# Optimization experiments

Measured on AMD Instinct MI355X. Metric: run time of the kernel, lower is better.

The kernel has to match this reference:

```python
import jax, jax.numpy as jnp
import numpy as np
from jax import lax

# ---- static config (matches init_kwargs: input_shape=(1,64,64), num_classes=2) ----
C, H, W = 1, 64, 64
NUM_CLASSES = 2
DIM_CAPS = 8          # primary capsule dim
NUM_PRIM = 32         # primary capsule types
OUT_DIM = 16          # class capsule dim
NUM_ROUTING = 3
HP = (H - 9) // 2 + 1  # 28  (9x9 conv, stride 2, no pad)
WP = (W - 9) // 2 + 1  # 28
IN_CAPS = NUM_PRIM * HP * WP  # 25088
TEMP_CH = 256 // H    # 4  channels after re-viewing temporal output
B = 32


def conv1d(x, w, b, pad):
    y = lax.conv_general_dilated(x, w, (1,), [(pad, pad)],
                                 dimension_numbers=('NCH', 'OIH', 'NCH'))
    return y + b[None, :, None]


def conv2d(x, w, b, stride, pad):
    y = lax.conv_general_dilated(x, w, (stride, stride), [(pad, pad), (pad, pad)],
                                 dimension_numbers=('NCHW', 'OIHW', 'NCHW'))
    return y + b[None, :, None, None]


def squash_vec(u):
    # proper capsule squash over last (dim_caps) axis -- used by PrimaryCapsule
    sn = jnp.sum(u * u, axis=-1, keepdims=True)
    return sn * u / ((1.0 + sn) * jnp.sqrt(sn + 1e-8))


def squash_elem(v):
    # RoutingCapsule squash: torch applies it over a trailing SINGLETON dim,
    # so it is elementwise: v^2 * v / ((1+v^2) * sqrt(v^2 + 1e-8))
    sn = v * v
    return sn * v / ((1.0 + sn) * jnp.sqrt(sn + 1e-8))


def setup_inputs() -> dict:
    key = jax.random.key(0)
    ks = jax.random.split(key, 20)
    s = 0.05
    inp = {
        'x':    jax.random.normal(ks[0], (B, C, H, W), dtype=jnp.float32),
        # temporal Conv1d stack (true in_channels = C*H = 64)
        'w_t1': jax.random.normal(ks[1], (64, C * H, 5), jnp.float32) * s,
        'b_t1': jnp.zeros((64,), jnp.float32),
        'w_t2': jax.random.normal(ks[2], (128, 64, 5), jnp.float32) * s,
        'b_t2': jnp.zeros((128,), jnp.float32),
        'w_t3': jax.random.normal(ks[3], (256, 128, 5), jnp.float32) * s,
        'b_t3': jnp.zeros((256,), jnp.float32),
        # spectral Conv2d stack
        'w_s1': jax.random.normal(ks[4], (64, C, 3, 3), jnp.float32) * s,
        'b_s1': jnp.zeros((64,), jnp.float32),
        'w_s2': jax.random.normal(ks[5], (128, 64, 3, 3), jnp.float32) * s,
        'b_s2': jnp.zeros((128,), jnp.float32),
        'w_s3': jax.random.normal(ks[6], (256, 128, 3, 3), jnp.float32) * s,
        'b_s3': jnp.zeros((256,), jnp.float32),
        # fusion 1x1 conv (in = 256/H + 256 = 260)
        'w_f':  jax.random.normal(ks[7], (256, TEMP_CH + 256, 1, 1), jnp.float32) * s,
        'b_f':  jnp.zeros((256,), jnp.float32),
        # primary capsule 9x9 stride-2 conv (out = 32*8 = 256)
        'w_p':  jax.random.normal(ks[8], (NUM_PRIM * DIM_CAPS, 256, 9, 9), jnp.float32) * s,
        'b_p':  jnp.zeros((NUM_PRIM * DIM_CAPS,), jnp.float32),
        # routing weight (torch: (1, in_caps, out_caps, out_dim, in_dim); leading 1 dropped)
        'w_r':  jax.random.normal(ks[9], (IN_CAPS, NUM_CLASSES, OUT_DIM, DIM_CAPS), jnp.float32) * s,
    }
    return inp


def reference(x, w_t1, b_t1, w_t2, b_t2, w_t3, b_t3,
              w_s1, b_s1, w_s2, b_s2, w_s3, b_s3,
              w_f, b_f, w_p, b_p, w_r):
    bsz = x.shape[0]
    # temporal branch: (B, C*H, W) -> Conv1d x3 -> (B, 256, W) -> (B, 256/H, H, W)
    xt = x.reshape(bsz, C * H, W)
    t = jax.nn.relu(conv1d(xt, w_t1, b_t1, 2))
    t = jax.nn.relu(conv1d(t, w_t2, b_t2, 2))
    t = jax.nn.relu(conv1d(t, w_t3, b_t3, 2))
    t = t.reshape(bsz, TEMP_CH, H, W)
    # spectral branch
    sp = jax.nn.relu(conv2d(x, w_s1, b_s1, 1, 1))
    sp = jax.nn.relu(conv2d(sp, w_s2, b_s2, 1, 1))
    sp = jax.nn.relu(conv2d(sp, w_s3, b_s3, 1, 1))
    # fuse
    fused = jnp.concatenate([t, sp], axis=1)          # (B, 260, H, W)
    fused = conv2d(fused, w_f, b_f, 1, 0)             # (B, 256, H, W)
    # primary capsules
    p = conv2d(fused, w_p, b_p, 2, 0)                 # (B, 256, HP, WP)
    p = p.reshape(bsz, NUM_PRIM, DIM_CAPS, HP * WP)
    p = jnp.transpose(p, (0, 1, 3, 2)).reshape(bsz, IN_CAPS, DIM_CAPS)
    u = squash_vec(p)                                 # (B, in_caps, 8)
    # dynamic routing
    u_hat = jnp.einsum('iodk,bik->biod', w_r, u)      # (B, in_caps, out_caps, out_dim)
    b_ij = jnp.zeros((bsz, IN_CAPS, NUM_CLASSES), dtype=u_hat.dtype)
    v = None
    for it in range(NUM_ROUTING):
        c = jax.nn.softmax(b_ij, axis=2)              # over out_caps
        s_j = jnp.einsum('bio,biod->bod', c, u_hat)   # (B, out_caps, out_dim)
        v = squash_elem(s_j)                          # elementwise (singleton-dim squash)
        if it < NUM_ROUTING - 1:
            b_ij = b_ij + jnp.einsum('biod,bod->bio', u_hat, v)
    # class_probs = (class_caps**2).sum(-1)**0.5 over a SINGLETON dim -> |v|
    return (v * v) ** 0.5                             # (B, num_classes, out_dim)
```

## Files before the change

### kernel.cpp

```cpp
#include <hip/hip_runtime.h>
#include <math.h>


#define BSZ 32

typedef unsigned short u16;
using bf16x8 = __attribute__((ext_vector_type(8))) short;
using f16x8 = __attribute__((ext_vector_type(8))) _Float16;
using f32x4 = __attribute__((ext_vector_type(4))) float;

__device__ inline u16 f2bf(float f) {
  union { float f; unsigned u; } v; v.f = f;
  unsigned r = v.u + 0x7FFF + ((v.u >> 16) & 1);
  return (u16)(r >> 16);
}
__device__ inline float bf2f(u16 h) {
  union { unsigned u; float f; } v; v.u = ((unsigned)h) << 16;
  return v.f;
}
__device__ inline u16 f2h(float f) {
  union { _Float16 h; u16 u; } v; v.h = (_Float16)f;
  return v.u;
}
__device__ inline float h2f(u16 b) {
  union { u16 u; _Float16 h; } v; v.u = b;
  return (float)v.h;
}

__global__ __launch_bounds__(256) void conv1d_relu_k(
    const float* __restrict__ in, const float* __restrict__ w,
    const float* __restrict__ bias, float* __restrict__ out, int CI, int CO) {
  int idx = blockIdx.x * 256 + threadIdx.x;
  int total = BSZ * CO * 64;
  if (idx >= total) return;
  int x = idx & 63;
  int co = (idx >> 6) % CO;
  int b = idx / (64 * CO);
  const float* ip = in + (size_t)b * CI * 64;
  const float* wp = w + (size_t)co * CI * 5;
  float acc = bias[co];
  for (int ci = 0; ci < CI; ++ci) {
    const float* ir = ip + ci * 64;
    const float* wr_ = wp + ci * 5;
#pragma unroll
    for (int k = 0; k < 5; ++k) {
      int xx = x + k - 2;
      if (xx >= 0 && xx < 64) acc += ir[xx] * wr_[k];
    }
  }
  out[idx] = fmaxf(acc, 0.f);
}

template <int CI, int CIC>
__global__ __launch_bounds__(256) void conv3x3_relu_k(
    const float* __restrict__ in, const float* __restrict__ w,
    const float* __restrict__ bias, float* __restrict__ out, int CO) {
  __shared__ float in_t[CIC][18][20];
  __shared__ float w_t[CIC][16][12];
  int t = threadIdx.x;
  int co_l = t & 15;
  int g = t >> 4;
  int gy = g >> 2, gx = g & 3;
  int y0 = (blockIdx.x >> 2) * 16, x0 = (blockIdx.x & 3) * 16;
  int co = blockIdx.y * 16 + co_l;
  int b = blockIdx.z;
  float acc[16];
#pragma unroll
  for (int i = 0; i < 16; ++i) acc[i] = 0.f;

  for (int cib = 0; cib < CI / CIC; ++cib) {
    int ci0 = cib * CIC;
    for (int s = t; s < CIC * 324; s += 256) {
      int ci = s / 324;
      int r = s - ci * 324;
      int iy = r / 18, ix = r - iy * 18;
      int gyy = y0 + iy - 1, gxx = x0 + ix - 1;
      float v = 0.f;
      if (gyy >= 0 && gyy < 64 && gxx >= 0 && gxx < 64)
        v = in[((size_t)b * CI + ci0 + ci) * 4096 + gyy * 64 + gxx];
      in_t[ci][iy][ix] = v;
    }
    for (int s = t; s < CIC * 144; s += 256) {
      int ci = s / 144;
      int r = s - ci * 144;
      int cw = r / 9, k = r - cw * 9;
      w_t[ci][cw][k] = w[((size_t)(blockIdx.y * 16 + cw) * CI + ci0 + ci) * 9 + k];
    }
    __syncthreads();
    for (int ci = 0; ci < CIC; ++ci) {
      float wv[9];
#pragma unroll
      for (int k = 0; k < 9; ++k) wv[k] = w_t[ci][co_l][k];
      float pin[36];
#pragma unroll
      for (int r6 = 0; r6 < 6; ++r6)
#pragma unroll
        for (int c6 = 0; c6 < 6; ++c6)
          pin[r6 * 6 + c6] = in_t[ci][4 * gy + r6][4 * gx + c6];
#pragma unroll
      for (int py = 0; py < 4; ++py)
#pragma unroll
        for (int px = 0; px < 4; ++px) {
          float s_ = acc[py * 4 + px];
#pragma unroll
          for (int ky = 0; ky < 3; ++ky)
#pragma unroll
            for (int kx = 0; kx < 3; ++kx)
              s_ += pin[(py + ky) * 6 + (px + kx)] * wv[ky * 3 + kx];
          acc[py * 4 + px] = s_;
        }
    }
    __syncthreads();
  }
  float bv = bias[co];
#pragma unroll
  for (int py = 0; py < 4; ++py)
#pragma unroll
    for (int px = 0; px < 4; ++px)
      out[((size_t)b * CO + co) * 4096 + (size_t)(y0 + 4 * gy + py) * 64 +
          (x0 + 4 * gx + px)] = fmaxf(acc[py * 4 + px] + bv, 0.f);
}

__global__ __launch_bounds__(256) void transpose_wf_k(const float* __restrict__ wf,
                                                      float* __restrict__ wfT) {
  int idx = blockIdx.x * 256 + threadIdx.x;
  if (idx >= 256 * 260) return;
  int co = idx / 260, c = idx - co * 260;
  wfT[c * 256 + co] = wf[idx];
}

__global__ __launch_bounds__(256) void transpose_wp_k(const float* __restrict__ wp,
                                                      u16* __restrict__ wth,
                                                      u16* __restrict__ wtl) {
  int s = blockIdx.x;
  int g = s / 81, t = s - g * 81;
  int co = threadIdx.x;
  u16 th[32], tl[32];
#pragma unroll
  for (int c = 0; c < 32; ++c) {
    float f = wp[((size_t)co * 256 + g * 32 + c) * 81 + t];
    u16 h = f2h(f);
    th[c] = h;
    tl[c] = f2h(f - h2f(h));
  }
  ushort4* dh = (ushort4*)(wth + ((size_t)s * 256 + co) * 32);
  ushort4* dl = (ushort4*)(wtl + ((size_t)s * 256 + co) * 32);
#pragma unroll
  for (int q = 0; q < 8; ++q) {
    dh[q] = make_ushort4(th[4 * q], th[4 * q + 1], th[4 * q + 2], th[4 * q + 3]);
    dl[q] = make_ushort4(tl[4 * q], tl[4 * q + 1], tl[4 * q + 2], tl[4 * q + 3]);
  }
}

template <int CO, int NCHUNK>
__global__ __launch_bounds__(256) void transpose_w3_k(const float* __restrict__ w,
                                                      u16* __restrict__ wh,
                                                      u16* __restrict__ wl) {
  int tab = blockIdx.x;
  int g = tab / 9, tap = tab - g * 9;
  int co = threadIdx.x;
  if (co >= CO) return;
  constexpr int CI = NCHUNK * 32;
  u16 th[32], tl[32];
#pragma unroll
  for (int c = 0; c < 32; ++c) {
    float f = w[((size_t)co * CI + g * 32 + c) * 9 + tap];
    u16 h = f2bf(f);
    th[c] = h;
    tl[c] = f2bf(f - bf2f(h));
  }
  ushort4* dh = (ushort4*)(wh + ((size_t)tab * CO + co) * 32);
  ushort4* dl = (ushort4*)(wl + ((size_t)tab * CO + co) * 32);
#pragma unroll
  for (int q = 0; q < 8; ++q) {
    dh[q] = make_ushort4(th[4 * q], th[4 * q + 1], th[4 * q + 2], th[4 * q + 3]);
    dl[q] = make_ushort4(tl[4 * q], tl[4 * q + 1], tl[4 * q + 2], tl[4 * q + 3]);
  }
}

template <int WMG, int WNG, int NCHUNK, int CO>
__global__ __launch_bounds__(512) void conv3x3_mfma_k(const float* __restrict__ in,
                                                      const u16* __restrict__ Wh,
                                                      const u16* __restrict__ Wl,
                                                      const float* __restrict__ bias,
                                                      float* __restrict__ out) {
  constexpr int CI = NCHUNK * 32;
  constexpr int ROWS = WMG + 2;
  __shared__ __align__(16) char lds_a[ROWS * 66 * 80];
  const int tid = threadIdx.x;
  const int b = blockIdx.y;
  const int y0 = blockIdx.x * WMG;
  const int w = tid >> 6, l = tid & 63;
  const int wm = w / WNG, wn = w % WNG;
  const int kb = l >> 4, il = l & 15;

  int abase[4];
#pragma unroll
  for (int mb = 0; mb < 4; ++mb) {
    int lp = (wm * 4 + mb) * 16 + il;
    int ly = lp >> 6, lx = lp & 63;
    abase[mb] = (ly * 66 + lx) * 80 + kb * 16;
  }
  int boff[4];
#pragma unroll
  for (int nbi = 0; nbi < 4; ++nbi)
    boff[nbi] = ((wn * 4 + nbi) * 16 + il) * 64 + kb * 16;

  f32x4 acc[4][4];
#pragma unroll
  for (int mb = 0; mb < 4; ++mb)
#pragma unroll
    for (int nbi = 0; nbi < 4; ++nbi) {
      f32x4 z = {0.f, 0.f, 0.f, 0.f};
      acc[mb][nbi] = z;
    }

  const float* Fb = in + (size_t)b * CI * 4096;
  const char* WhB = (const char*)Wh;
  const char* WlB = (const char*)Wl;

  auto stageA = [&](int g, int plane) {
    const float* src = Fb + (size_t)g * 32 * 4096;
    for (int s = tid; s < ROWS * 66 * 8; s += 512) {
      int ciq = s & 7;
      int rest = s >> 3;
      int r = rest / 66, x = rest - r * 66;
      int row = y0 - 1 + r, col = x - 1;
      float a0 = 0.f, a1 = 0.f, a2 = 0.f, a3 = 0.f;
      if (row >= 0 && row < 64 && col >= 0 && col < 64) {
        const float* p = src + (size_t)(ciq * 4) * 4096 + row * 64 + col;
        a0 = p[0];
        a1 = p[4096];
        a2 = p[8192];
        a3 = p[12288];
      }
      u16 e0, e1, e2, e3;
      if (plane == 0) {
        e0 = f2bf(a0); e1 = f2bf(a1); e2 = f2bf(a2); e3 = f2bf(a3);
      } else {
        u16 h0 = f2bf(a0), h1 = f2bf(a1), h2 = f2bf(a2), h3 = f2bf(a3);
        e0 = f2bf(a0 - bf2f(h0)); e1 = f2bf(a1 - bf2f(h1));
        e2 = f2bf(a2 - bf2f(h2)); e3 = f2bf(a3 - bf2f(h3));
      }
      *(ushort4*)(lds_a + (r * 66 + x) * 80 + ciq * 8) = make_ushort4(e0, e1, e2, e3);
    }
  };

  for (int g = 0; g < NCHUNK; ++g) {
    __syncthreads();
    stageA(g, 0);
    __syncthreads();
#pragma unroll
    for (int tap = 0; tap < 9; ++tap) {
      const char* pb = WhB + (size_t)(g * 9 + tap) * (CO * 64);
      const char* pl = WlB + (size_t)(g * 9 + tap) * (CO * 64);
      bf16x8 bh[4], bl[4];
#pragma unroll
      for (int nbi = 0; nbi < 4; ++nbi) {
        bh[nbi] = *(const bf16x8*)(pb + boff[nbi]);
        bl[nbi] = *(const bf16x8*)(pl + boff[nbi]);
      }
      int ky = tap / 3, kx = tap - ky * 3;
      int toff = (ky * 66 + kx) * 80;
      bf16x8 av[4];
#pragma unroll
      for (int mb = 0; mb < 4; ++mb)
        av[mb] = *(const bf16x8*)(lds_a + abase[mb] + toff);
#pragma unroll
      for (int mb = 0; mb < 4; ++mb)
#pragma unroll
        for (int nbi = 0; nbi < 4; ++nbi) {
          acc[mb][nbi] = __builtin_amdgcn_mfma_f32_16x16x32_bf16(
              av[mb], bh[nbi], acc[mb][nbi], 0, 0, 0);
          acc[mb][nbi] = __builtin_amdgcn_mfma_f32_16x16x32_bf16(
              av[mb], bl[nbi], acc[mb][nbi], 0, 0, 0);
        }
    }
    __syncthreads();
    stageA(g, 1);
    __syncthreads();
#pragma unroll
    for (int tap = 0; tap < 9; ++tap) {
      const char* pb = WhB + (size_t)(g * 9 + tap) * (CO * 64);
      bf16x8 bh[4];
#pragma unroll
      for (int nbi = 0; nbi < 4; ++nbi)
        bh[nbi] = *(const bf16x8*)(pb + boff[nbi]);
      int ky = tap / 3, kx = tap - ky * 3;
      int toff = (ky * 66 + kx) * 80;
      bf16x8 av[4];
#pragma unroll
      for (int mb = 0; mb < 4; ++mb)
        av[mb] = *(const bf16x8*)(lds_a + abase[mb] + toff);
#pragma unroll
      for (int mb = 0; mb < 4; ++mb)
#pragma unroll
        for (int nbi = 0; nbi < 4; ++nbi)
          acc[mb][nbi] = __builtin_amdgcn_mfma_f32_16x16x32_bf16(
              av[mb], bh[nbi], acc[mb][nbi], 0, 0, 0);
    }
  }

  const int p0 = y0 * 64;
#pragma unroll
  for (int mb = 0; mb < 4; ++mb) {
    int pixb = p0 + (wm * 4 + mb) * 16 + kb * 4;
#pragma unroll
    for (int nbi = 0; nbi < 4; ++nbi) {
      int co = (wn * 4 + nbi) * 16 + il;
      float bv_ = bias[co];
      f32x4 a = acc[mb][nbi];
      float4 o = make_float4(fmaxf(a[0] + bv_, 0.f), fmaxf(a[1] + bv_, 0.f),
                             fmaxf(a[2] + bv_, 0.f), fmaxf(a[3] + bv_, 0.f));
      *(float4*)(out + (size_t)(b * CO + co) * 4096 + pixb) = o;
    }
  }
}

__global__ __launch_bounds__(256) void fuse1x1_k(const float* __restrict__ t3,
                                                 const float* __restrict__ wfT,
                                                 const float* __restrict__ bf,
                                                 float* __restrict__ a) {
  __shared__ float in_t[260][32];
  int t = threadIdx.x;
  int b = blockIdx.x >> 7;
  int p0 = (blockIdx.x & 127) * 32;
  for (int s = t; s < 260 * 32; s += 256) {
    int c = s >> 5, pp = s & 31;
    float v;
    if (c < 4)
      v = t3[(size_t)b * 16384 + c * 4096 + p0 + pp];
    else
      v = a[((size_t)b * 256 + (c - 4)) * 4096 + p0 + pp];
    in_t[c][pp] = v;
  }
  __syncthreads();
  int co = t;
  float acc[32];
#pragma unroll
  for (int pp = 0; pp < 32; ++pp) acc[pp] = 0.f;
  for (int c = 0; c < 260; ++c) {
    float wv = wfT[c * 256 + co];
#pragma unroll
    for (int pp = 0; pp < 32; ++pp) acc[pp] += wv * in_t[c][pp];
  }
  float bv = bf[co];
#pragma unroll
  for (int pp = 0; pp < 32; ++pp)
    a[((size_t)b * 256 + co) * 4096 + p0 + pp] = acc[pp] + bv;
}

__global__ __launch_bounds__(1024) void conv9x9_mfma_k(const float* __restrict__ fused,
                                                       const u16* __restrict__ WTh,
                                                       const u16* __restrict__ WTl,
                                                       const float* __restrict__ bias,
                                                       float* __restrict__ praw) {
  constexpr int APLANE = 19 * 32 * 80;
  __shared__ __align__(16) char lds_a[2 * APLANE];
  const int tid = threadIdx.x;
  const int b = blockIdx.y, tile = blockIdx.x;
  const int p0 = tile * 128;
  const int oy0 = p0 / 28;
  const int w = tid >> 6, l = tid & 63;
  const int wm = w >> 3, wn = w & 7;
  const int kb = l >> 4, il = l & 15;

  int abase[4];
#pragma unroll
  for (int mb = 0; mb < 4; ++mb) {
    int p = p0 + (wm * 4 + mb) * 16 + il;
    int oy = p / 28, ox = p - oy * 28;
    abase[mb] = (2 * (oy - oy0)) * 2560 + ox * 80 + kb * 16;
  }
  int boff[2];
#pragma unroll
  for (int nbi = 0; nbi < 2; ++nbi)
    boff[nbi] = (wn * 32 + nbi * 16 + il) * 64 + kb * 16;

  f32x4 acc[4][2];
#pragma unroll
  for (int mb = 0; mb < 4; ++mb)
#pragma unroll
    for (int nbi = 0; nbi < 2; ++nbi) {
      f32x4 z = {0.f, 0.f, 0.f, 0.f};
      acc[mb][nbi] = z;
    }

  const float* Fb = fused + (size_t)b * 256 * 4096;
  const char* WhB = (const char*)WTh;
  const char* WlB = (const char*)WTl;

  auto stageA = [&](int g) {
    const float* src = Fb + (size_t)g * 32 * 4096;
    for (int s = tid; s < 19 * 63 * 8; s += 1024) {
      int ciq = s / 1197;
      int rem = s - ciq * 1197;
      int r = rem / 63, t63 = rem - r * 63;
      int x2 = (t63 < 32) ? 2 * t63 : 2 * (t63 - 32) + 1;
      int iy = 2 * oy0 + r;
      float a0 = 0.f, a1 = 0.f, a2 = 0.f, a3 = 0.f;
      if (iy < 64) {
        const float* pp0 = src + (size_t)(ciq * 4) * 4096 + iy * 64 + x2;
        a0 = pp0[0];
        a1 = pp0[4096];
        a2 = pp0[8192];
        a3 = pp0[12288];
      }
      u16 e0 = f2h(a0), e1 = f2h(a1), e2 = f2h(a2), e3 = f2h(a3);
      int off = (x2 & 1) * APLANE + (r * 32 + (x2 >> 1)) * 80 + ciq * 8;
      *(ushort4*)(lds_a + off) = make_ushort4(e0, e1, e2, e3);
    }
  };

  for (int g = 0; g < 8; ++g) {
    __syncthreads();
    stageA(g);
    __syncthreads();
#pragma unroll 3
    for (int t = 0; t < 81; ++t) {
      const char* pb = WhB + (size_t)(g * 81 + t) * 16384;
      const char* pl = WlB + (size_t)(g * 81 + t) * 16384;
      f16x8 bh[2], bl[2];
#pragma unroll
      for (int nbi = 0; nbi < 2; ++nbi) {
        bh[nbi] = *(const f16x8*)(pb + boff[nbi]);
        bl[nbi] = *(const f16x8*)(pl + boff[nbi]);
      }
      int ky = t / 9, kx = t - ky * 9;
      int toff = (kx & 1) * APLANE + ky * 2560 + (kx >> 1) * 80;
      f16x8 av[4];
#pragma unroll
      for (int mb = 0; mb < 4; ++mb)
        av[mb] = *(const f16x8*)(lds_a + abase[mb] + toff);
#pragma unroll
      for (int mb = 0; mb < 4; ++mb)
#pragma unroll
        for (int nbi = 0; nbi < 2; ++nbi) {
          acc[mb][nbi] = __builtin_amdgcn_mfma_f32_16x16x32_f16(
              av[mb], bh[nbi], acc[mb][nbi], 0, 0, 0);
          acc[mb][nbi] = __builtin_amdgcn_mfma_f32_16x16x32_f16(
              av[mb], bl[nbi], acc[mb][nbi], 0, 0, 0);
        }
    }
  }

#pragma unroll
  for (int mb = 0; mb < 4; ++mb) {
    int pixb = p0 + (wm * 4 + mb) * 16 + kb * 4;
    if (pixb < 784) {
#pragma unroll
      for (int nbi = 0; nbi < 2; ++nbi) {
        int co = wn * 32 + nbi * 16 + il;
        float bv_ = bias[co];
        f32x4 a = acc[mb][nbi];
        float4 o = make_float4(a[0] + bv_, a[1] + bv_, a[2] + bv_, a[3] + bv_);
        *(float4*)(praw + (size_t)(b * 256 + co) * 784 + pixb) = o;
      }
    }
  }
}

__global__ __launch_bounds__(256) void squash_caps_k(const float* __restrict__ p,
                                                     float* __restrict__ u) {
  int idx = blockIdx.x * 256 + threadIdx.x;
  if (idx >= BSZ * 25088) return;
  int b = idx / 25088;
  int cap = idx - b * 25088;
  int prim = cap / 784, pix = cap - prim * 784;
  const float* pp = p + ((size_t)b * 256 + prim * 8) * 784 + pix;
  float x[8];
  float sn = 0.f;
#pragma unroll
  for (int d = 0; d < 8; ++d) {
    x[d] = pp[(size_t)d * 784];
    sn += x[d] * x[d];
  }
  float scale = sn / ((1.f + sn) * sqrtf(sn + 1e-8f));
  float4 r0 = {x[0] * scale, x[1] * scale, x[2] * scale, x[3] * scale};
  float4 r1 = {x[4] * scale, x[5] * scale, x[6] * scale, x[7] * scale};
  float4* dst = (float4*)(u + (size_t)idx * 8);
  dst[0] = r0;
  dst[1] = r1;
}

__global__ __launch_bounds__(256) void uhat_k(const float* __restrict__ u,
                                              const float* __restrict__ w_r,
                                              float* __restrict__ u_hat) {
  int i = blockIdx.x * 256 + threadIdx.x;
  int b = blockIdx.y;
  const float4* up = (const float4*)(u + ((size_t)b * 25088 + i) * 8);
  float4 ua = up[0], ub = up[1];
  const float4* wr = (const float4*)(w_r + (size_t)i * 256);
  float res[32];
#pragma unroll
  for (int od = 0; od < 32; ++od) {
    float4 wa = wr[od * 2], wb = wr[od * 2 + 1];
    res[od] = wa.x * ua.x + wa.y * ua.y + wa.z * ua.z + wa.w * ua.w +
              wb.x * ub.x + wb.y * ub.y + wb.z * ub.z + wb.w * ub.w;
  }
  float4* dst = (float4*)(u_hat + ((size_t)b * 25088 + i) * 32);
#pragma unroll
  for (int q = 0; q < 8; ++q)
    dst[q] = make_float4(res[4 * q], res[4 * q + 1], res[4 * q + 2], res[4 * q + 3]);
}

__global__ __launch_bounds__(256) void route_sj_k(const float* __restrict__ u_hat,
                                                  const float* __restrict__ b_ij,
                                                  float* __restrict__ sj_part, int iter) {
  int b = blockIdx.x;
  int seg = blockIdx.y;
  int t = threadIdx.x;
  float acc[32];
#pragma unroll
  for (int j = 0; j < 32; ++j) acc[j] = 0.f;
  int i0 = seg * 3136;
  for (int i = i0 + t; i < i0 + 3136; i += 256) {
    float c0 = 0.5f, c1 = 0.5f;
    if (iter > 0) {
      float b0 = b_ij[((size_t)b * 25088 + i) * 2 + 0];
      float b1 = b_ij[((size_t)b * 25088 + i) * 2 + 1];
      float m = fmaxf(b0, b1);
      float e0 = expf(b0 - m), e1 = expf(b1 - m);
      float inv = 1.f / (e0 + e1);
      c0 = e0 * inv;
      c1 = e1 * inv;
    }
    const float4* uh = (const float4*)(u_hat + ((size_t)b * 25088 + i) * 32);
#pragma unroll
    for (int q = 0; q < 4; ++q) {
      float4 va = uh[q];
      acc[4 * q + 0] += c0 * va.x;
      acc[4 * q + 1] += c0 * va.y;
      acc[4 * q + 2] += c0 * va.z;
      acc[4 * q + 3] += c0 * va.w;
      float4 vb = uh[4 + q];
      acc[16 + 4 * q + 0] += c1 * vb.x;
      acc[16 + 4 * q + 1] += c1 * vb.y;
      acc[16 + 4 * q + 2] += c1 * vb.z;
      acc[16 + 4 * q + 3] += c1 * vb.w;
    }
  }
#pragma unroll
  for (int j = 0; j < 32; ++j) {
    acc[j] += __shfl_down(acc[j], 32);
    acc[j] += __shfl_down(acc[j], 16);
    acc[j] += __shfl_down(acc[j], 8);
    acc[j] += __shfl_down(acc[j], 4);
    acc[j] += __shfl_down(acc[j], 2);
    acc[j] += __shfl_down(acc[j], 1);
  }
  __shared__ float red[4][32];
  int wave = t >> 6, lane = t & 63;
  if (lane == 0) {
#pragma unroll
    for (int j = 0; j < 32; ++j) red[wave][j] = acc[j];
  }
  __syncthreads();
  if (t < 32) {
    float s = red[0][t] + red[1][t] + red[2][t] + red[3][t];
    sj_part[((size_t)b * 8 + seg) * 32 + t] = s;
  }
}

__global__ __launch_bounds__(256) void route_fin_k(const float* __restrict__ sj_part,
                                                   float* __restrict__ v,
                                                   float* __restrict__ out, int final_it) {
  int idx = blockIdx.x * 256 + threadIdx.x;
  if (idx >= BSZ * 32) return;
  int b = idx >> 5, j = idx & 31;
  float s = 0.f;
#pragma unroll
  for (int seg = 0; seg < 8; ++seg) s += sj_part[((size_t)b * 8 + seg) * 32 + j];
  float sn = s * s;
  float vv = sn * s / ((1.f + sn) * sqrtf(sn + 1e-8f));
  v[idx] = vv;
  if (final_it) out[idx] = fabsf(vv);
}

__global__ __launch_bounds__(256) void route_upd_k(const float* __restrict__ u_hat,
                                                   const float* __restrict__ v,
                                                   float* __restrict__ b_ij, int first) {
  int i = blockIdx.x * 256 + threadIdx.x;
  int b = blockIdx.y;
  const float4* uh = (const float4*)(u_hat + ((size_t)b * 25088 + i) * 32);
  const float4* vp = (const float4*)(v + b * 32);
  float e0 = 0.f, e1 = 0.f;
#pragma unroll
  for (int q = 0; q < 4; ++q) {
    float4 a = uh[q], wv = vp[q];
    e0 += a.x * wv.x + a.y * wv.y + a.z * wv.z + a.w * wv.w;
    float4 a2 = uh[4 + q], w2 = vp[4 + q];
    e1 += a2.x * w2.x + a2.y * w2.y + a2.z * w2.z + a2.w * w2.w;
  }
  size_t o = ((size_t)b * 25088 + i) * 2;
  if (first) {
    b_ij[o + 0] = e0;
    b_ij[o + 1] = e1;
  } else {
    b_ij[o + 0] += e0;
    b_ij[o + 1] += e1;
  }
}

extern "C" void kernel_launch(void* const* d_in, const int* in_sizes, int n_in,
                              void* d_out, int out_size, void* d_ws, size_t ws_size,
                              hipStream_t stream) {
  (void)in_sizes; (void)n_in; (void)out_size;
  const float* x    = (const float*)d_in[0];
  const float* w_t1 = (const float*)d_in[1];
  const float* b_t1 = (const float*)d_in[2];
  const float* w_t2 = (const float*)d_in[3];
  const float* b_t2 = (const float*)d_in[4];
  const float* w_t3 = (const float*)d_in[5];
  const float* b_t3 = (const float*)d_in[6];
  const float* w_s1 = (const float*)d_in[7];
  const float* b_s1 = (const float*)d_in[8];
  const float* w_s2 = (const float*)d_in[9];
  const float* b_s2 = (const float*)d_in[10];
  const float* w_s3 = (const float*)d_in[11];
  const float* b_s3 = (const float*)d_in[12];
  const float* w_f  = (const float*)d_in[13];
  const float* b_f  = (const float*)d_in[14];
  const float* w_p  = (const float*)d_in[15];
  const float* b_p  = (const float*)d_in[16];
  const float* w_r  = (const float*)d_in[17];
  float* out = (float*)d_out;

  char* ws = (char*)d_ws;
  if (ws_size < 238854144ull) return;
  float* fused = (float*)(ws + 0);
  float* uhat  = (float*)(ws + 0);
  float* s2q   = (float*)(ws + 134217728);
  float* praw  = (float*)(ws + 134217728);
  float* u     = (float*)(ws + 159907840);
  float* b_ij  = (float*)(ws + 185597952);
  float* s1    = (float*)(ws + 201326592);
  float* t1    = (float*)(ws + 201326592);
  float* t2    = (float*)(ws + 201850880);
  float* t3    = (float*)(ws + 202899456);
  u16*   wTh   = (u16*)  (ws + 204996608);
  u16*   wTl   = (u16*)  (ws + 215613440);
  u16*   w3a_h = (u16*)  (ws + 234881024);
  u16*   w3a_l = (u16*)  (ws + 235028480);
  u16*   w3b_h = (u16*)  (ws + 235175936);
  u16*   w3b_l = (u16*)  (ws + 235765760);
  float* wfT   = (float*)(ws + 236355584);
  float* sjp   = (float*)(ws + 236621824);
  float* vbuf  = (float*)(ws + 236654592);

  transpose_w3_k<128, 2><<<18, 256, 0, stream>>>(w_s2, w3a_h, w3a_l);
  transpose_w3_k<256, 4><<<36, 256, 0, stream>>>(w_s3, w3b_h, w3b_l);
  transpose_wf_k<<<261, 256, 0, stream>>>(w_f, wfT);

  conv3x3_relu_k<1, 1><<<dim3(16, 4, BSZ), 256, 0, stream>>>(x, w_s1, b_s1, s1, 64);
  conv3x3_mfma_k<4, 2, 2, 128><<<dim3(16, BSZ), 512, 0, stream>>>(s1, w3a_h, w3a_l, b_s2, s2q);

  conv1d_relu_k<<<512, 256, 0, stream>>>(x, w_t1, b_t1, t1, 64, 64);
  conv1d_relu_k<<<1024, 256, 0, stream>>>(t1, w_t2, b_t2, t2, 64, 128);
  conv1d_relu_k<<<2048, 256, 0, stream>>>(t2, w_t3, b_t3, t3, 128, 256);
  transpose_wp_k<<<648, 256, 0, stream>>>(w_p, wTh, wTl);

  conv3x3_mfma_k<2, 4, 4, 256><<<dim3(32, BSZ), 512, 0, stream>>>(s2q, w3b_h, w3b_l, b_s3, fused);

  fuse1x1_k<<<4096, 256, 0, stream>>>(t3, wfT, b_f, fused);

  conv9x9_mfma_k<<<dim3(7, BSZ), 1024, 0, stream>>>(fused, wTh, wTl, b_p, praw);
  squash_caps_k<<<3136, 256, 0, stream>>>(praw, u);

  uhat_k<<<dim3(98, BSZ), 256, 0, stream>>>(u, w_r, uhat);

  route_sj_k<<<dim3(BSZ, 8), 256, 0, stream>>>(uhat, b_ij, sjp, 0);
  route_fin_k<<<4, 256, 0, stream>>>(sjp, vbuf, out, 0);
  route_upd_k<<<dim3(98, BSZ), 256, 0, stream>>>(uhat, vbuf, b_ij, 1);

  route_sj_k<<<dim3(BSZ, 8), 256, 0, stream>>>(uhat, b_ij, sjp, 1);
  route_fin_k<<<4, 256, 0, stream>>>(sjp, vbuf, out, 0);
  route_upd_k<<<dim3(98, BSZ), 256, 0, stream>>>(uhat, vbuf, b_ij, 0);

  route_sj_k<<<dim3(BSZ, 8), 256, 0, stream>>>(uhat, b_ij, sjp, 2);
  route_fin_k<<<4, 256, 0, stream>>>(sjp, vbuf, out, 1);
}
```

Before: 1.774 ms.

## Move 1x1 fuse conv to split-bf16 MFMA and fuse routing update into s_j pass

Replaces the scalar FP32 1x1 fusion convolution with an MFMA kernel that splits activations and weights into bf16 high/low parts and uses three products to keep near-FP32 accuracy. The weight transpose now emits packed bf16 hi/lo tiles. Separately, the routing logit update is folded into the next s_j reduction pass, so u_hat is read once per iteration instead of twice. It also specialises the first s_j pass to the uniform 0.5 coupling. The costs are a small precision loss from dropping the low-times-low term and in-place reads and writes of the fused buffer inside the GEMM.

```diff
diff --git a/kernel.cpp b/kernel.cpp
--- a/kernel.cpp
+++ b/kernel.cpp
@@ -121,12 +121,27 @@
           (x0 + 4 * gx + px)] = fmaxf(acc[py * 4 + px] + bv, 0.f);
 }
 
-__global__ __launch_bounds__(256) void transpose_wf_k(const float* __restrict__ wf,
-                                                      float* __restrict__ wfT) {
-  int idx = blockIdx.x * 256 + threadIdx.x;
-  if (idx >= 256 * 260) return;
-  int co = idx / 260, c = idx - co * 260;
-  wfT[c * 256 + co] = wf[idx];
+__global__ __launch_bounds__(256) void transpose_wf1_k(const float* __restrict__ wf,
+                                                       u16* __restrict__ wh,
+                                                       u16* __restrict__ wl) {
+  int c = blockIdx.x;
+  int co = threadIdx.x;
+  u16 th[32], tl[32];
+#pragma unroll
+  for (int j = 0; j < 32; ++j) {
+    int lc = c * 32 + j;
+    float f = (lc < 260) ? wf[(size_t)co * 260 + lc] : 0.f;
+    u16 h = f2bf(f);
+    th[j] = h;
+    tl[j] = f2bf(f - bf2f(h));
+  }
+  ushort4* dh = (ushort4*)(wh + ((size_t)c * 256 + co) * 32);
+  ushort4* dl = (ushort4*)(wl + ((size_t)c * 256 + co) * 32);
+#pragma unroll
+  for (int q = 0; q < 8; ++q) {
+    dh[q] = make_ushort4(th[4 * q], th[4 * q + 1], th[4 * q + 2], th[4 * q + 3]);
+    dl[q] = make_ushort4(tl[4 * q], tl[4 * q + 1], tl[4 * q + 2], tl[4 * q + 3]);
+  }
 }
 
 __global__ __launch_bounds__(256) void transpose_wp_k(const float* __restrict__ wp,
@@ -317,37 +332,105 @@
   }
 }
 
-__global__ __launch_bounds__(256) void fuse1x1_k(const float* __restrict__ t3,
-                                                 const float* __restrict__ wfT,
-                                                 const float* __restrict__ bf,
-                                                 float* __restrict__ a) {
-  __shared__ float in_t[260][32];
-  int t = threadIdx.x;
-  int b = blockIdx.x >> 7;
-  int p0 = (blockIdx.x & 127) * 32;
-  for (int s = t; s < 260 * 32; s += 256) {
-    int c = s >> 5, pp = s & 31;
-    float v;
-    if (c < 4)
-      v = t3[(size_t)b * 16384 + c * 4096 + p0 + pp];
-    else
-      v = a[((size_t)b * 256 + (c - 4)) * 4096 + p0 + pp];
-    in_t[c][pp] = v;
-  }
-  __syncthreads();
-  int co = t;
-  float acc[32];
-#pragma unroll
-  for (int pp = 0; pp < 32; ++pp) acc[pp] = 0.f;
-  for (int c = 0; c < 260; ++c) {
-    float wv = wfT[c * 256 + co];
-#pragma unroll
-    for (int pp = 0; pp < 32; ++pp) acc[pp] += wv * in_t[c][pp];
-  }
-  float bv = bf[co];
-#pragma unroll
-  for (int pp = 0; pp < 32; ++pp)
-    a[((size_t)b * 256 + co) * 4096 + p0 + pp] = acc[pp] + bv;
+__global__ __launch_bounds__(512) void fuse_mfma_k(const float* __restrict__ t3,
+                                                   const u16* __restrict__ Wh,
+                                                   const u16* __restrict__ Wl,
+                                                   const float* __restrict__ bf,
+                                                   float* __restrict__ a) {
+  constexpr int APL = 128 * 80;
+  __shared__ __align__(16) char lds_a[2 * APL];
+  const int tid = threadIdx.x;
+  const int b = blockIdx.y;
+  const int p0 = blockIdx.x * 128;
+  const int w = tid >> 6, l = tid & 63;
+  const int wm = w >> 2, wn = w & 3;
+  const int kb = l >> 4, il = l & 15;
+
+  int abase[4];
+#pragma unroll
+  for (int mb = 0; mb < 4; ++mb)
+    abase[mb] = ((wm * 4 + mb) * 16 + il) * 80 + kb * 16;
+  int boff[4];
+#pragma unroll
+  for (int nbi = 0; nbi < 4; ++nbi)
+    boff[nbi] = ((wn * 4 + nbi) * 16 + il) * 64 + kb * 16;
+
+  f32x4 acc[4][4];
+#pragma unroll
+  for (int mb = 0; mb < 4; ++mb)
+#pragma unroll
+    for (int nbi = 0; nbi < 4; ++nbi) {
+      f32x4 z = {0.f, 0.f, 0.f, 0.f};
+      acc[mb][nbi] = z;
+    }
+
+  const char* WhB = (const char*)Wh;
+  const char* WlB = (const char*)Wl;
+
+  auto stageAB = [&](int c) {
+    for (int s = tid; s < 128 * 8; s += 512) {
+      int ciq = s & 7, px = s >> 3;
+      int pg = p0 + px;
+      u16 eh[4], el[4];
+#pragma unroll
+      for (int q = 0; q < 4; ++q) {
+        int lc = c * 32 + ciq * 4 + q;
+        float f = 0.f;
+        if (lc < 4)
+          f = t3[(size_t)b * 16384 + lc * 4096 + pg];
+        else if (lc < 260)
+          f = a[((size_t)b * 256 + (lc - 4)) * 4096 + pg];
+        u16 h = f2bf(f);
+        eh[q] = h;
+        el[q] = f2bf(f - bf2f(h));
+      }
+      *(ushort4*)(lds_a + px * 80 + ciq * 8) = make_ushort4(eh[0], eh[1], eh[2], eh[3]);
+      *(ushort4*)(lds_a + APL + px * 80 + ciq * 8) =
+          make_ushort4(el[0], el[1], el[2], el[3]);
+    }
+  };
+
+  for (int c = 0; c < 9; ++c) {
+    __syncthreads();
+    stageAB(c);
+    __syncthreads();
+    bf16x8 bh[4], bl[4];
+#pragma unroll
+    for (int nbi = 0; nbi < 4; ++nbi) {
+      bh[nbi] = *(const bf16x8*)(WhB + (size_t)c * 16384 + boff[nbi]);
+      bl[nbi] = *(const bf16x8*)(WlB + (size_t)c * 16384 + boff[nbi]);
+    }
+    bf16x8 avh[4], avl[4];
+#pragma unroll
+    for (int mb = 0; mb < 4; ++mb) {
+      avh[mb] = *(const bf16x8*)(lds_a + abase[mb]);
+      avl[mb] = *(const bf16x8*)(lds_a + APL + abase[mb]);
+    }
+#pragma unroll
+    for (int mb = 0; mb < 4; ++mb)
+#pragma unroll
+      for (int nbi = 0; nbi < 4; ++nbi) {
+        acc[mb][nbi] = __builtin_amdgcn_mfma_f32_16x16x32_bf16(
+            avh[mb], bh[nbi], acc[mb][nbi], 0, 0, 0);
+        acc[mb][nbi] = __builtin_amdgcn_mfma_f32_16x16x32_bf16(
+            avh[mb], bl[nbi], acc[mb][nbi], 0, 0, 0);
+        acc[mb][nbi] = __builtin_amdgcn_mfma_f32_16x16x32_bf16(
+            avl[mb], bh[nbi], acc[mb][nbi], 0, 0, 0);
+      }
+  }
+
+#pragma unroll
+  for (int mb = 0; mb < 4; ++mb) {
+    int pixb = p0 + (wm * 4 + mb) * 16 + kb * 4;
+#pragma unroll
+    for (int nbi = 0; nbi < 4; ++nbi) {
+      int co = (wn * 4 + nbi) * 16 + il;
+      float bv_ = bf[co];
+      f32x4 v = acc[mb][nbi];
+      float4 o = make_float4(v[0] + bv_, v[1] + bv_, v[2] + bv_, v[3] + bv_);
+      *(float4*)(a + (size_t)(b * 256 + co) * 4096 + pixb) = o;
+    }
+  }
 }
 
 __global__ __launch_bounds__(1024) void conv9x9_mfma_k(const float* __restrict__ fused,
@@ -452,8 +535,8 @@
       for (int nbi = 0; nbi < 2; ++nbi) {
         int co = wn * 32 + nbi * 16 + il;
         float bv_ = bias[co];
-        f32x4 a = acc[mb][nbi];
-        float4 o = make_float4(a[0] + bv_, a[1] + bv_, a[2] + bv_, a[3] + bv_);
+        f32x4 v = acc[mb][nbi];
+        float4 o = make_float4(v[0] + bv_, v[1] + bv_, v[2] + bv_, v[3] + bv_);
         *(float4*)(praw + (size_t)(b * 256 + co) * 784 + pixb) = o;
       }
     }
@@ -505,8 +588,7 @@
 }
 
 __global__ __launch_bounds__(256) void route_sj_k(const float* __restrict__ u_hat,
-                                                  const float* __restrict__ b_ij,
-                                                  float* __restrict__ sj_part, int iter) {
+                                                  float* __restrict__ sj_part) {
   int b = blockIdx.x;
   int seg = blockIdx.y;
   int t = threadIdx.x;
@@ -515,29 +597,19 @@
   for (int j = 0; j < 32; ++j) acc[j] = 0.f;
   int i0 = seg * 3136;
   for (int i = i0 + t; i < i0 + 3136; i += 256) {
-    float c0 = 0.5f, c1 = 0.5f;
-    if (iter > 0) {
-      float b0 = b_ij[((size_t)b * 25088 + i) * 2 + 0];
-      float b1 = b_ij[((size_t)b * 25088 + i) * 2 + 1];
-      float m = fmaxf(b0, b1);
-      float e0 = expf(b0 - m), e1 = expf(b1 - m);
-      float inv = 1.f / (e0 + e1);
-      c0 = e0 * inv;
-      c1 = e1 * inv;
-    }
     const float4* uh = (const float4*)(u_hat + ((size_t)b * 25088 + i) * 32);
 #pragma unroll
     for (int q = 0; q < 4; ++q) {
       float4 va = uh[q];
-      acc[4 * q + 0] += c0 * va.x;
-      acc[4 * q + 1] += c0 * va.y;
-      acc[4 * q + 2] += c0 * va.z;
-      acc[4 * q + 3] += c0 * va.w;
+      acc[4 * q + 0] += 0.5f * va.x;
+      acc[4 * q + 1] += 0.5f * va.y;
+      acc[4 * q + 2] += 0.5f * va.z;
+      acc[4 * q + 3] += 0.5f * va.w;
       float4 vb = uh[4 + q];
-      acc[16 + 4 * q + 0] += c1 * vb.x;
-      acc[16 + 4 * q + 1] += c1 * vb.y;
-      acc[16 + 4 * q + 2] += c1 * vb.z;
-      acc[16 + 4 * q + 3] += c1 * vb.w;
+      acc[16 + 4 * q + 0] += 0.5f * vb.x;
+      acc[16 + 4 * q + 1] += 0.5f * vb.y;
+      acc[16 + 4 * q + 2] += 0.5f * vb.z;
+      acc[16 + 4 * q + 3] += 0.5f * vb.w;
     }
   }
 #pragma unroll
@@ -562,6 +634,82 @@
   }
 }
 
+__global__ __launch_bounds__(256) void route_fsj_k(const float* __restrict__ u_hat,
+                                                   const float* __restrict__ v,
+                                                   float* __restrict__ b_ij,
+                                                   float* __restrict__ sj_part, int first) {
+  int b = blockIdx.x;
+  int seg = blockIdx.y;
+  int t = threadIdx.x;
+  float4 vp[8];
+  const float4* vv = (const float4*)(v + b * 32);
+#pragma unroll
+  for (int q = 0; q < 8; ++q) vp[q] = vv[q];
+  float acc[32];
+#pragma unroll
+  for (int j = 0; j < 32; ++j) acc[j] = 0.f;
+  int i0 = seg * 3136;
+  for (int i = i0 + t; i < i0 + 3136; i += 256) {
+    const float4* uhp = (const float4*)(u_hat + ((size_t)b * 25088 + i) * 32);
+    float4 uh[8];
+#pragma unroll
+    for (int q = 0; q < 8; ++q) uh[q] = uhp[q];
+    float e0 = 0.f, e1 = 0.f;
+#pragma unroll
+    for (int q = 0; q < 4; ++q) {
+      e0 += uh[q].x * vp[q].x + uh[q].y * vp[q].y + uh[q].z * vp[q].z + uh[q].w * vp[q].w;
+      e1 += uh[4 + q].x * vp[4 + q].x + uh[4 + q].y * vp[4 + q].y +
+            uh[4 + q].z * vp[4 + q].z + uh[4 + q].w * vp[4 + q].w;
+    }
+    size_t o = ((size_t)b * 25088 + i) * 2;
+    float b0, b1;
+    if (first) {
+      b0 = e0;
+      b1 = e1;
+      b_ij[o + 0] = e0;
+      b_ij[o + 1] = e1;
+    } else {
+      b0 = b_ij[o + 0] + e0;
+      b1 = b_ij[o + 1] + e1;
+    }
+    float m = fmaxf(b0, b1);
+    float x0 = expf(b0 - m), x1 = expf(b1 - m);
+    float inv = 1.f / (x0 + x1);
+    float c0 = x0 * inv, c1 = x1 * inv;
+#pragma unroll
+    for (int q = 0; q < 4; ++q) {
+      acc[4 * q + 0] += c0 * uh[q].x;
+      acc[4 * q + 1] += c0 * uh[q].y;
+      acc[4 * q + 2] += c0 * uh[q].z;
+      acc[4 * q + 3] += c0 * uh[q].w;
+      acc[16 + 4 * q + 0] += c1 * uh[4 + q].x;
+      acc[16 + 4 * q + 1] += c1 * uh[4 + q].y;
+      acc[16 + 4 * q + 2] += c1 * uh[4 + q].z;
+      acc[16 + 4 * q + 3] += c1 * uh[4 + q].w;
+    }
+  }
+#pragma unroll
+  for (int j = 0; j < 32; ++j) {
+    acc[j] += __shfl_down(acc[j], 32);
+    acc[j] += __shfl_down(acc[j], 16);
+    acc[j] += __shfl_down(acc[j], 8);
+    acc[j] += __shfl_down(acc[j], 4);
+    acc[j] += __shfl_down(acc[j], 2);
+    acc[j] += __shfl_down(acc[j], 1);
+  }
+  __shared__ float red[4][32];
+  int wave = t >> 6, lane = t & 63;
+  if (lane == 0) {
+#pragma unroll
+    for (int j = 0; j < 32; ++j) red[wave][j] = acc[j];
+  }
+  __syncthreads();
+  if (t < 32) {
+    float s = red[0][t] + red[1][t] + red[2][t] + red[3][t];
+    sj_part[((size_t)b * 8 + seg) * 32 + t] = s;
+  }
+}
+
 __global__ __launch_bounds__(256) void route_fin_k(const float* __restrict__ sj_part,
                                                    float* __restrict__ v,
                                                    float* __restrict__ out, int final_it) {
@@ -575,31 +723,6 @@
   float vv = sn * s / ((1.f + sn) * sqrtf(sn + 1e-8f));
   v[idx] = vv;
   if (final_it) out[idx] = fabsf(vv);
-}
-
-__global__ __launch_bounds__(256) void route_upd_k(const float* __restrict__ u_hat,
-                                                   const float* __restrict__ v,
-                                                   float* __restrict__ b_ij, int first) {
-  int i = blockIdx.x * 256 + threadIdx.x;
-  int b = blockIdx.y;
-  const float4* uh = (const float4*)(u_hat + ((size_t)b * 25088 + i) * 32);
-  const float4* vp = (const float4*)(v + b * 32);
-  float e0 = 0.f, e1 = 0.f;
-#pragma unroll
-  for (int q = 0; q < 4; ++q) {
-    float4 a = uh[q], wv = vp[q];
-    e0 += a.x * wv.x + a.y * wv.y + a.z * wv.z + a.w * wv.w;
-    float4 a2 = uh[4 + q], w2 = vp[4 + q];
-    e1 += a2.x * w2.x + a2.y * w2.y + a2.z * w2.z + a2.w * w2.w;
-  }
-  size_t o = ((size_t)b * 25088 + i) * 2;
-  if (first) {
-    b_ij[o + 0] = e0;
-    b_ij[o + 1] = e1;
-  } else {
-    b_ij[o + 0] += e0;
-    b_ij[o + 1] += e1;
-  }
 }
 
 extern "C" void kernel_launch(void* const* d_in, const int* in_sizes, int n_in,
@@ -644,13 +767,14 @@
   u16*   w3a_l = (u16*)  (ws + 235028480);
   u16*   w3b_h = (u16*)  (ws + 235175936);
   u16*   w3b_l = (u16*)  (ws + 235765760);
-  float* wfT   = (float*)(ws + 236355584);
-  float* sjp   = (float*)(ws + 236621824);
-  float* vbuf  = (float*)(ws + 236654592);
+  u16*   wf1_h = (u16*)  (ws + 236355584);
+  u16*   wf1_l = (u16*)  (ws + 236503040);
+  float* sjp   = (float*)(ws + 236650496);
+  float* vbuf  = (float*)(ws + 236683264);
 
   transpose_w3_k<128, 2><<<18, 256, 0, stream>>>(w_s2, w3a_h, w3a_l);
   transpose_w3_k<256, 4><<<36, 256, 0, stream>>>(w_s3, w3b_h, w3b_l);
-  transpose_wf_k<<<261, 256, 0, stream>>>(w_f, wfT);
+  transpose_wf1_k<<<9, 256, 0, stream>>>(w_f, wf1_h, wf1_l);
 
   conv3x3_relu_k<1, 1><<<dim3(16, 4, BSZ), 256, 0, stream>>>(x, w_s1, b_s1, s1, 64);
   conv3x3_mfma_k<4, 2, 2, 128><<<dim3(16, BSZ), 512, 0, stream>>>(s1, w3a_h, w3a_l, b_s2, s2q);
@@ -662,21 +786,17 @@
 
   conv3x3_mfma_k<2, 4, 4, 256><<<dim3(32, BSZ), 512, 0, stream>>>(s2q, w3b_h, w3b_l, b_s3, fused);
 
-  fuse1x1_k<<<4096, 256, 0, stream>>>(t3, wfT, b_f, fused);
+  fuse_mfma_k<<<dim3(32, BSZ), 512, 0, stream>>>(t3, wf1_h, wf1_l, b_f, fused);
 
   conv9x9_mfma_k<<<dim3(7, BSZ), 1024, 0, stream>>>(fused, wTh, wTl, b_p, praw);
   squash_caps_k<<<3136, 256, 0, stream>>>(praw, u);
 
   uhat_k<<<dim3(98, BSZ), 256, 0, stream>>>(u, w_r, uhat);
 
-  route_sj_k<<<dim3(BSZ, 8), 256, 0, stream>>>(uhat, b_ij, sjp, 0);
+  route_sj_k<<<dim3(BSZ, 8), 256, 0, stream>>>(uhat, sjp);
   route_fin_k<<<4, 256, 0, stream>>>(sjp, vbuf, out, 0);
-  route_upd_k<<<dim3(98, BSZ), 256, 0, stream>>>(uhat, vbuf, b_ij, 1);
-
-  route_sj_k<<<dim3(BSZ, 8), 256, 0, stream>>>(uhat, b_ij, sjp, 1);
+  route_fsj_k<<<dim3(BSZ, 8), 256, 0, stream>>>(uhat, vbuf, b_ij, sjp, 1);
   route_fin_k<<<4, 256, 0, stream>>>(sjp, vbuf, out, 0);
-  route_upd_k<<<dim3(98, BSZ), 256, 0, stream>>>(uhat, vbuf, b_ij, 0);
-
-  route_sj_k<<<dim3(BSZ, 8), 256, 0, stream>>>(uhat, b_ij, sjp, 2);
+  route_fsj_k<<<dim3(BSZ, 8), 256, 0, stream>>>(uhat, vbuf, b_ij, sjp, 0);
   route_fin_k<<<4, 256, 0, stream>>>(sjp, vbuf, out, 1);
 }
```

Result: faster. 1.560 ms (-12.1%).
